# Kernel optimization log

Measured on AMD Instinct MI355X. Metric: run time of the kernel, lower is better.

## Reference

```python
import jax, jax.numpy as jnp
import numpy as np

B, C, H, W = 8, 256, 64, 64
GROUPS = 16
EPS = 1e-6


def setup_inputs() -> dict:
    key = jax.random.key(0)
    ks = jax.random.split(key, 11)
    s = 1.0 / np.sqrt(C)
    return {
        "x": jax.random.normal(ks[0], (B, C, H, W), dtype=jnp.float32),
        "norm_w": jnp.ones((C,), dtype=jnp.float32),
        "norm_b": jnp.zeros((C,), dtype=jnp.float32),
        "wq": jax.random.normal(ks[1], (C, C), dtype=jnp.float32) * s,
        "bq": jnp.zeros((C,), dtype=jnp.float32),
        "wk": jax.random.normal(ks[2], (C, C), dtype=jnp.float32) * s,
        "bk": jnp.zeros((C,), dtype=jnp.float32),
        "wv": jax.random.normal(ks[3], (C, C), dtype=jnp.float32) * s,
        "bv": jnp.zeros((C,), dtype=jnp.float32),
        "wp": jax.random.normal(ks[4], (C, C), dtype=jnp.float32) * s,
        "bp": jnp.zeros((C,), dtype=jnp.float32),
    }


def _conv1x1(h, w, b):
    # 1x1 conv == per-pixel linear over channels; w: [out_c, in_c]
    return jnp.einsum('bchw,oc->bohw', h, w) + b[None, :, None, None]


def reference(x, norm_w, norm_b, wq, bq, wk, bk, wv, bv, wp, bp):
    b, c, h, w = x.shape
    n = h * w
    # GroupNorm(16 groups, eps=1e-6, affine)
    xg = x.reshape(b, GROUPS, c // GROUPS, h, w)
    mu = xg.mean(axis=(2, 3, 4), keepdims=True)
    var = xg.var(axis=(2, 3, 4), keepdims=True)
    hn = ((xg - mu) * jax.lax.rsqrt(var + EPS)).reshape(b, c, h, w)
    hn = hn * norm_w[None, :, None, None] + norm_b[None, :, None, None]
    # QKV via 1x1 convs
    q = _conv1x1(hn, wq, bq).reshape(b, c, n)  # b c n
    k = _conv1x1(hn, wk, bk).reshape(b, c, n)
    v = _conv1x1(hn, wv, bv).reshape(b, c, n)
    # attention: scores [b, n, n], softmax over keys (last axis)
    att = jnp.einsum('bci,bcj->bij', q, k) * (c ** -0.5)
    att = jax.nn.softmax(att, axis=2)
    # h_[b,c,i] = sum_j v[b,c,j] * att[b,i,j]
    out = jnp.einsum('bcj,bij->bci', v, att).reshape(b, c, h, w)
    return x + _conv1x1(out, wp, bp)
```

## Files before the change

kernel.cpp:

```cpp
#include <hip/hip_runtime.h>


#define B_ 8
#define C_ 256
#define NPIX 4096

typedef short short8v __attribute__((ext_vector_type(8)));
typedef unsigned short ush4 __attribute__((ext_vector_type(4)));
typedef float f32x16 __attribute__((ext_vector_type(16)));

__device__ __forceinline__ unsigned short f2bf(float f) {
  unsigned u = __builtin_bit_cast(unsigned, f);
  u += 0x7fffu + ((u >> 16) & 1u);
  return (unsigned short)(u >> 16);
}

__device__ __forceinline__ void gload_lds16(const void* g, void* l) {
  __builtin_amdgcn_global_load_lds((const __attribute__((address_space(1))) void*)g,
                                   (__attribute__((address_space(3))) void*)l, 16, 0, 0);
}

__global__ __launch_bounds__(256)
void gn_part(const float4* __restrict__ x4, float* __restrict__ part) {
  const int bg = blockIdx.x >> 3;
  const int sl = blockIdx.x & 7;
  const float4* xp = x4 + (size_t)bg * (16 * NPIX / 4) + sl * 128;
  float s = 0.f, ss = 0.f;
  #pragma unroll
  for (int u = 0; u < 8; ++u) {
    const int idx = u * 256 + threadIdx.x;
    float4 v = xp[(size_t)(idx >> 7) * (NPIX / 4) + (idx & 127)];
    s  += v.x + v.y + v.z + v.w;
    ss += v.x * v.x + v.y * v.y + v.z * v.z + v.w * v.w;
  }
  #pragma unroll
  for (int off = 32; off; off >>= 1) { s += __shfl_down(s, off); ss += __shfl_down(ss, off); }
  __shared__ float sm1[4], sm2[4];
  const int w = threadIdx.x >> 6, l = threadIdx.x & 63;
  if (l == 0) { sm1[w] = s; sm2[w] = ss; }
  __syncthreads();
  if (threadIdx.x == 0) {
    part[blockIdx.x * 2]     = sm1[0] + sm1[1] + sm1[2] + sm1[3];
    part[blockIdx.x * 2 + 1] = sm2[0] + sm2[1] + sm2[2] + sm2[3];
  }
}

__global__ __launch_bounds__(128)
void gn_fin(const float* __restrict__ part, float* __restrict__ stats) {
  const int t = threadIdx.x;
  float s = 0.f, ss = 0.f;
  #pragma unroll
  for (int p = 0; p < 8; ++p) { s += part[(t * 8 + p) * 2]; ss += part[(t * 8 + p) * 2 + 1]; }
  const float mean = s * (1.f / 65536.f);
  const float var  = ss * (1.f / 65536.f) - mean * mean;
  stats[t * 2]     = mean;
  stats[t * 2 + 1] = rsqrtf(var + 1e-6f);
}

template <int MODE>
__global__ __launch_bounds__(256, 2)
void gemm_k(const float* __restrict__ Wa, const float* __restrict__ ba,
            const float* __restrict__ Wb, const float* __restrict__ bb,
            const float* __restrict__ x, const float* __restrict__ stats,
            const float* __restrict__ gamma, const float* __restrict__ beta,
            const unsigned short* __restrict__ aT,
            unsigned short* __restrict__ dq, unsigned short* __restrict__ dk,
            float* __restrict__ dout) {
  extern __shared__ __align__(16) unsigned char sm[];
  unsigned char* sX = sm;
  unsigned char* sW = sm + 32768;
  float* sscl = (float*)(sm + 65536);
  float* ssh  = sscl + 256;

  const int t = threadIdx.x;
  const int w = t >> 6, l = t & 63, hi = l >> 5, ln = l & 31;
  const int b  = blockIdx.z;
  const int n0 = blockIdx.x * 128;
  const int o0 = blockIdx.y * 128;

  const float* Wsel = (MODE == 0 && o0 >= 256) ? Wb : Wa;
  const float* bsel = (MODE == 0 && o0 >= 256) ? bb : ba;
  const int orow0 = o0 & 255;

  if (MODE < 2) {
    const int c = t;
    const float mean = stats[(b * 16 + (c >> 4)) * 2];
    const float rstd = stats[(b * 16 + (c >> 4)) * 2 + 1];
    const float sl = rstd * gamma[c];
    sscl[c] = sl; ssh[c] = beta[c] - mean * sl;
  }
  __syncthreads();

  const float* xb = x + (size_t)b * C_ * NPIX;
  const unsigned short* aTb = aT + (size_t)b * NPIX * C_;

  auto stage = [&](int s) {
    const int c0 = s * 64;
    unsigned char* Xb_ = sX + (s & 1) * 16384;
    unsigned char* Wb_ = sW + (s & 1) * 16384;
    #pragma unroll
    for (int i = 0; i < 8; ++i) {
      const int idx = i * 256 + t;
      const int o = idx >> 4;
      const int cq = (idx & 15) * 4;
      float4 v = *(const float4*)&Wsel[(size_t)(orow0 + o) * C_ + c0 + cq];
      ush4 h; h[0] = f2bf(v.x); h[1] = f2bf(v.y); h[2] = f2bf(v.z); h[3] = f2bf(v.w);
      *(ush4*)(Wb_ + ((o * 128 + cq * 2) ^ ((o & 7) << 4))) = h;
    }
    if (MODE < 2) {
      const int co = t & 7, q = t >> 3;
      float vv[8][4];
      #pragma unroll
      for (int i = 0; i < 8; ++i) {
        const int c = c0 + 8 * co + i;
        float4 v = *(const float4*)&xb[(size_t)c * NPIX + n0 + 4 * q];
        const float slc = sscl[c], shc = ssh[c];
        vv[i][0] = v.x * slc + shc; vv[i][1] = v.y * slc + shc;
        vv[i][2] = v.z * slc + shc; vv[i][3] = v.w * slc + shc;
      }
      #pragma unroll
      for (int nn = 0; nn < 4; ++nn) {
        short8v h;
        #pragma unroll
        for (int j = 0; j < 8; ++j) h[j] = (short)f2bf(vv[j][nn]);
        const int n = 4 * q + nn;
        *(short8v*)(Xb_ + ((n * 128 + 16 * co) ^ ((n & 7) << 4))) = h;
      }
    } else {
      const int cs = t & 7, nb = t >> 3;
      #pragma unroll
      for (int r = 0; r < 4; ++r) {
        const int n = nb + 32 * r;
        short8v v = *(const short8v*)&aTb[(size_t)(n0 + n) * C_ + c0 + 8 * cs];
        *(short8v*)(Xb_ + ((n * 128 + 16 * cs) ^ ((n & 7) << 4))) = v;
      }
    }
  };

  f32x16 acc[2][2];
  #pragma unroll
  for (int i = 0; i < 2; ++i)
    #pragma unroll
    for (int j = 0; j < 2; ++j)
      #pragma unroll
      for (int r = 0; r < 16; ++r) acc[i][j][r] = 0.f;

  stage(0);
  __syncthreads();
  for (int s = 0; s < 4; ++s) {
    if (s < 3) stage(s + 1);
    const unsigned char* Xb_ = sX + (s & 1) * 16384;
    const unsigned char* Wb_ = sW + (s & 1) * 16384;
    #pragma unroll
    for (int ks = 0; ks < 4; ++ks) {
      short8v xa[2], wf[2];
      #pragma unroll
      for (int mt = 0; mt < 2; ++mt) {
        const int n = 64 * (w >> 1) + 32 * mt + ln;
        xa[mt] = *(const short8v*)(Xb_ + ((n * 128 + 32 * ks + 16 * hi) ^ ((n & 7) << 4)));
        const int o = 64 * (w & 1) + 32 * mt + ln;
        wf[mt] = *(const short8v*)(Wb_ + ((o * 128 + 32 * ks + 16 * hi) ^ ((o & 7) << 4)));
      }
      #pragma unroll
      for (int mt = 0; mt < 2; ++mt)
        #pragma unroll
        for (int nt = 0; nt < 2; ++nt)
          acc[mt][nt] = (MODE == 0)
            ? __builtin_amdgcn_mfma_f32_32x32x16_bf16(xa[mt], wf[nt], acc[mt][nt], 0, 0, 0)
            : __builtin_amdgcn_mfma_f32_32x32x16_bf16(wf[mt], xa[nt], acc[mt][nt], 0, 0, 0);
    }
    __syncthreads();
  }

  if (MODE == 0) {
    unsigned short* dst = (o0 < 256) ? dq : dk;
    const float scv = (o0 < 256) ? 0.0625f : 1.0f;
    #pragma unroll
    for (int nt = 0; nt < 2; ++nt) {
      const int o = o0 + 64 * (w & 1) + 32 * nt + ln;
      const float bi = bsel[o & 255];
      #pragma unroll
      for (int mt = 0; mt < 2; ++mt)
        #pragma unroll
        for (int r = 0; r < 16; ++r) {
          const int n = n0 + 64 * (w >> 1) + 32 * mt + (r & 3) + 8 * (r >> 2) + 4 * hi;
          dst[((size_t)b * NPIX + n) * C_ + (o & 255)] = f2bf((acc[mt][nt][r] + bi) * scv);
        }
    }
  } else if (MODE == 1) {
    #pragma unroll
    for (int nt = 0; nt < 2; ++nt) {
      const int n = n0 + 64 * (w >> 1) + 32 * nt + ln;
      #pragma unroll
      for (int mt = 0; mt < 2; ++mt)
        #pragma unroll
        for (int r = 0; r < 16; ++r) {
          const int o = o0 + 64 * (w & 1) + 32 * mt + (r & 3) + 8 * (r >> 2) + 4 * hi;
          dq[((size_t)b * C_ + o) * NPIX + n] = f2bf(acc[mt][nt][r] + ba[o]);
        }
    }
  } else {
    #pragma unroll
    for (int nt = 0; nt < 2; ++nt) {
      const int n = n0 + 64 * (w >> 1) + 32 * nt + ln;
      #pragma unroll
      for (int mt = 0; mt < 2; ++mt)
        #pragma unroll
        for (int r = 0; r < 16; ++r) {
          const int o = o0 + 64 * (w & 1) + 32 * mt + (r & 3) + 8 * (r >> 2) + 4 * hi;
          const size_t ad = ((size_t)b * C_ + o) * NPIX + n;
          dout[ad] = acc[mt][nt][r] + ba[o] + x[ad];
        }
    }
  }
}

__global__ __launch_bounds__(256, 1)
void attn_k(const unsigned short* __restrict__ qt,
            const unsigned short* __restrict__ kt,
            const unsigned short* __restrict__ vb,
            unsigned short* __restrict__ aT) {
  extern __shared__ __align__(16) unsigned char smem[];
  const int t = threadIdx.x;
  const int w = t >> 6, l = t & 63, hi = l >> 5, ln = l & 31;
  const int bid = blockIdx.x;
  const int b = bid & 7;
  const int i0 = (bid >> 3) * 128;

  const size_t nc = (size_t)NPIX * C_;
  const unsigned short* qb  = qt + (size_t)b * nc;
  const unsigned char*  kbb = (const unsigned char*)(kt + (size_t)b * nc);
  const unsigned char*  vbb = (const unsigned char*)(vb + (size_t)b * nc);

  const unsigned short* qrow = qb + (size_t)(i0 + 32 * w + ln) * C_ + 8 * hi;
  short8v qf[16];
  #pragma unroll
  for (int cs = 0; cs < 16; ++cs) qf[cs] = *(const short8v*)(qrow + 16 * cs);

  f32x16 Ot[8];
  #pragma unroll
  for (int ct = 0; ct < 8; ++ct)
    #pragma unroll
    for (int r = 0; r < 16; ++r) Ot[ct][r] = 0.f;
  float m_r = -3.0e38f, l_r = 0.f;

  auto stage = [&](int buf, int j0) {
    unsigned char* Kd = smem + buf * 32768;
    unsigned char* Vd = smem + 65536 + buf * 32768;
    #pragma unroll
    for (int u = 0; u < 8; ++u) {
      const int p = w * 8192 + u * 1024 + l * 16;
      const int j = p >> 9;
      const int inner = (p & 511) ^ ((j & 7) << 4);
      gload_lds16(kbb + (size_t)(j0 + j) * 512 + inner, Kd + w * 8192 + u * 1024);
    }
    #pragma unroll
    for (int u = 0; u < 8; ++u) {
      const int p = w * 8192 + u * 1024 + l * 16;
      const int c = p >> 7;
      const int inner = (p & 127) ^ ((c & 7) << 4);
      gload_lds16(vbb + (size_t)c * 8192 + j0 * 2 + inner, Vd + w * 8192 + u * 1024);
    }
  };

  stage(0, 0);
  __syncthreads();

  for (int it = 0; it < 64; ++it) {
    const int cur = it & 1;
    if (it < 63) stage(cur ^ 1, (it + 1) * 64);

    const unsigned char* Kb = smem + cur * 32768;
    f32x16 st0, st1;
    #pragma unroll
    for (int r = 0; r < 16; ++r) { st0[r] = 0.f; st1[r] = 0.f; }
    #pragma unroll
    for (int cs = 0; cs < 16; ++cs) {
      const int cb = 32 * cs + 16 * hi;
      short8v kf0 = *(const short8v*)(Kb + ((ln * 512 + cb) ^ ((ln & 7) << 4)));
      st0 = __builtin_amdgcn_mfma_f32_32x32x16_bf16(kf0, qf[cs], st0, 0, 0, 0);
      short8v kf1 = *(const short8v*)(Kb + (((32 + ln) * 512 + cb) ^ ((ln & 7) << 4)));
      st1 = __builtin_amdgcn_mfma_f32_32x32x16_bf16(kf1, qf[cs], st1, 0, 0, 0);
    }

    float mt = st0[0];
    #pragma unroll
    for (int r = 1; r < 16; ++r) mt = fmaxf(mt, st0[r]);
    #pragma unroll
    for (int r = 0; r < 16; ++r) mt = fmaxf(mt, st1[r]);
    mt = fmaxf(mt, __shfl_xor(mt, 32));
    const float mnew = fmaxf(m_r, mt);
    const float sc = __expf(m_r - mnew);
    m_r = mnew;
    float rs = 0.f;
    #pragma unroll
    for (int r = 0; r < 16; ++r) { st0[r] = __expf(st0[r] - mnew); rs += st0[r]; }
    #pragma unroll
    for (int r = 0; r < 16; ++r) { st1[r] = __expf(st1[r] - mnew); rs += st1[r]; }
    rs += __shfl_xor(rs, 32);
    l_r = l_r * sc + rs;
    #pragma unroll
    for (int ct = 0; ct < 8; ++ct) Ot[ct] *= sc;

    short8v pf[4];
    #pragma unroll
    for (int g = 0; g < 4; ++g) {
      f32x16 sv = (g < 2) ? st0 : st1;
      const int rb = (g & 1) * 8;
      unsigned pk01, pk23, pk45, pk67;
      asm("v_cvt_pk_bf16_f32 %0, %1, %2" : "=v"(pk01) : "v"(sv[rb + 0]), "v"(sv[rb + 1]));
      asm("v_cvt_pk_bf16_f32 %0, %1, %2" : "=v"(pk23) : "v"(sv[rb + 2]), "v"(sv[rb + 3]));
      asm("v_cvt_pk_bf16_f32 %0, %1, %2" : "=v"(pk45) : "v"(sv[rb + 4]), "v"(sv[rb + 5]));
      asm("v_cvt_pk_bf16_f32 %0, %1, %2" : "=v"(pk67) : "v"(sv[rb + 6]), "v"(sv[rb + 7]));
      asm volatile("v_permlane32_swap_b32 %0, %1" : "+v"(pk01), "+v"(pk45));
      asm volatile("v_permlane32_swap_b32 %0, %1" : "+v"(pk23), "+v"(pk67));
      int4 fi = {(int)pk01, (int)pk23, (int)pk45, (int)pk67};
      pf[g] = __builtin_bit_cast(short8v, fi);
    }

    const unsigned char* Vbuf = smem + 65536 + cur * 32768;
    #pragma unroll
    for (int ks = 0; ks < 4; ++ks) {
      #pragma unroll
      for (int ct = 0; ct < 8; ++ct) {
        const int c = 32 * ct + ln;
        short8v vf = *(const short8v*)(Vbuf + ((c * 128 + 32 * ks + 16 * hi) ^ ((c & 7) << 4)));
        Ot[ct] = __builtin_amdgcn_mfma_f32_32x32x16_bf16(vf, pf[ks], Ot[ct], 0, 0, 0);
      }
    }
    __syncthreads();
  }

  const float rinv = 1.0f / l_r;
  const int iloc = 32 * w + ln;
  #pragma unroll
  for (int ct = 0; ct < 8; ++ct) {
    #pragma unroll
    for (int h = 0; h < 2; ++h) {
      const int rb = h * 8;
      unsigned pk01, pk23, pk45, pk67;
      float q0 = Ot[ct][rb + 0] * rinv, q1 = Ot[ct][rb + 1] * rinv;
      float q2 = Ot[ct][rb + 2] * rinv, q3 = Ot[ct][rb + 3] * rinv;
      float q4 = Ot[ct][rb + 4] * rinv, q5 = Ot[ct][rb + 5] * rinv;
      float q6 = Ot[ct][rb + 6] * rinv, q7 = Ot[ct][rb + 7] * rinv;
      asm("v_cvt_pk_bf16_f32 %0, %1, %2" : "=v"(pk01) : "v"(q0), "v"(q1));
      asm("v_cvt_pk_bf16_f32 %0, %1, %2" : "=v"(pk23) : "v"(q2), "v"(q3));
      asm("v_cvt_pk_bf16_f32 %0, %1, %2" : "=v"(pk45) : "v"(q4), "v"(q5));
      asm("v_cvt_pk_bf16_f32 %0, %1, %2" : "=v"(pk67) : "v"(q6), "v"(q7));
      asm volatile("v_permlane32_swap_b32 %0, %1" : "+v"(pk01), "+v"(pk45));
      asm volatile("v_permlane32_swap_b32 %0, %1" : "+v"(pk23), "+v"(pk67));
      int4 fi = {(int)pk01, (int)pk23, (int)pk45, (int)pk67};
      const int byte = (iloc * 512 + 64 * ct + 32 * h + 16 * hi) ^ ((iloc & 7) << 4);
      *(short8v*)(smem + byte) = __builtin_bit_cast(short8v, fi);
    }
  }
  __syncthreads();
  unsigned char* aTb = (unsigned char*)(aT + ((size_t)b * NPIX + i0) * C_);
  #pragma unroll
  for (int p = 0; p < 16; ++p) {
    const int idx = p * 256 + t;
    const int il = idx >> 5, ch = idx & 31;
    const int byte = (il * 512 + ch * 16) ^ ((il & 7) << 4);
    *(short8v*)(aTb + il * 512 + ch * 16) = *(const short8v*)(smem + byte);
  }
}

extern "C" void kernel_launch(void* const* d_in, const int* in_sizes, int n_in,
                              void* d_out, int out_size, void* d_ws, size_t ws_size,
                              hipStream_t stream) {
  (void)in_sizes; (void)n_in; (void)out_size; (void)ws_size;
  const float* x      = (const float*)d_in[0];
  const float* norm_w = (const float*)d_in[1];
  const float* norm_b = (const float*)d_in[2];
  const float* wq = (const float*)d_in[3];
  const float* bq = (const float*)d_in[4];
  const float* wk = (const float*)d_in[5];
  const float* bk = (const float*)d_in[6];
  const float* wv = (const float*)d_in[7];
  const float* bv = (const float*)d_in[8];
  const float* wp = (const float*)d_in[9];
  const float* bp = (const float*)d_in[10];
  float* out = (float*)d_out;

  unsigned char* ws = (unsigned char*)d_ws;
  float* part  = (float*)ws;
  float* stats = (float*)(ws + 8192);
  unsigned short* qtb = (unsigned short*)(ws + 65536);
  unsigned short* ktb = qtb + (size_t)8 * 1024 * 1024;
  unsigned short* vbb = ktb + (size_t)8 * 1024 * 1024;
  unsigned short* aTb = vbb + (size_t)8 * 1024 * 1024;

  hipFuncSetAttribute((const void*)gemm_k<0>, hipFuncAttributeMaxDynamicSharedMemorySize, 67584);
  hipFuncSetAttribute((const void*)gemm_k<1>, hipFuncAttributeMaxDynamicSharedMemorySize, 67584);
  hipFuncSetAttribute((const void*)gemm_k<2>, hipFuncAttributeMaxDynamicSharedMemorySize, 67584);
  hipFuncSetAttribute((const void*)attn_k,    hipFuncAttributeMaxDynamicSharedMemorySize, 131072);

  gn_part<<<1024, 256, 0, stream>>>((const float4*)x, part);
  gn_fin<<<1, 128, 0, stream>>>(part, stats);

  gemm_k<0><<<dim3(32, 4, B_), 256, 67584, stream>>>(wq, bq, wk, bk, x, stats, norm_w, norm_b,
                                                     nullptr, qtb, ktb, nullptr);
  gemm_k<1><<<dim3(32, 2, B_), 256, 67584, stream>>>(wv, bv, nullptr, nullptr, x, stats, norm_w, norm_b,
                                                     nullptr, vbb, nullptr, nullptr);

  attn_k<<<256, 256, 131072, stream>>>(qtb, ktb, vbb, aTb);

  gemm_k<2><<<dim3(32, 2, B_), 256, 67584, stream>>>(wp, bp, nullptr, nullptr, x, nullptr, nullptr, nullptr,
                                                     aTb, nullptr, nullptr, out);
}
```

Baseline: 392.7 us.

## Split attention over key halves, fuse QKV GEMMs, add combine kernel

The Q/K/V projections now run in one kernel, and their outputs are staged through LDS so global stores are coalesced. Attention splits the key range into two halves (512 blocks, 2 blocks/CU, smaller K/V tiles). It switches to exp2 with log2e folded into the Q scale and skips the output rescale when the running max grows by less than a threshold. A new combine kernel merges the partial outputs and writes the bf16 transposed result, aiming to fill the GPU better. The cost is an extra fp32 partial-output round trip through memory and one more kernel launch.

```diff
diff --git a/kernel.cpp b/kernel.cpp
--- a/kernel.cpp
+++ b/kernel.cpp
@@ -7,6 +7,7 @@
 
 typedef short short8v __attribute__((ext_vector_type(8)));
 typedef unsigned short ush4 __attribute__((ext_vector_type(4)));
+typedef unsigned short ush8 __attribute__((ext_vector_type(8)));
 typedef float f32x16 __attribute__((ext_vector_type(16)));
 
 __device__ __forceinline__ unsigned short f2bf(float f) {
@@ -57,15 +58,14 @@
   stats[t * 2 + 1] = rsqrtf(var + 1e-6f);
 }
 
-template <int MODE>
 __global__ __launch_bounds__(256, 2)
-void gemm_k(const float* __restrict__ Wa, const float* __restrict__ ba,
-            const float* __restrict__ Wb, const float* __restrict__ bb,
-            const float* __restrict__ x, const float* __restrict__ stats,
-            const float* __restrict__ gamma, const float* __restrict__ beta,
-            const unsigned short* __restrict__ aT,
-            unsigned short* __restrict__ dq, unsigned short* __restrict__ dk,
-            float* __restrict__ dout) {
+void qkv_k(const float* __restrict__ wq, const float* __restrict__ bq,
+           const float* __restrict__ wk, const float* __restrict__ bk,
+           const float* __restrict__ wv, const float* __restrict__ bv,
+           const float* __restrict__ x, const float* __restrict__ stats,
+           const float* __restrict__ gamma, const float* __restrict__ beta,
+           unsigned short* __restrict__ qt, unsigned short* __restrict__ kt,
+           unsigned short* __restrict__ vo) {
   extern __shared__ __align__(16) unsigned char sm[];
   unsigned char* sX = sm;
   unsigned char* sW = sm + 32768;
@@ -76,13 +76,13 @@
   const int w = t >> 6, l = t & 63, hi = l >> 5, ln = l & 31;
   const int b  = blockIdx.z;
   const int n0 = blockIdx.x * 128;
-  const int o0 = blockIdx.y * 128;
-
-  const float* Wsel = (MODE == 0 && o0 >= 256) ? Wb : Wa;
-  const float* bsel = (MODE == 0 && o0 >= 256) ? bb : ba;
-  const int orow0 = o0 & 255;
-
-  if (MODE < 2) {
+  const int y  = blockIdx.y;
+  const bool vmode = (y >= 4);
+  const float* W   = (y < 2) ? wq : ((y < 4) ? wk : wv);
+  const float* bia = (y < 2) ? bq : ((y < 4) ? bk : bv);
+  const int o0 = (y & 1) * 128;
+
+  {
     const int c = t;
     const float mean = stats[(b * 16 + (c >> 4)) * 2];
     const float rstd = stats[(b * 16 + (c >> 4)) * 2 + 1];
@@ -92,7 +92,6 @@
   __syncthreads();
 
   const float* xb = x + (size_t)b * C_ * NPIX;
-  const unsigned short* aTb = aT + (size_t)b * NPIX * C_;
 
   auto stage = [&](int s) {
     const int c0 = s * 64;
@@ -103,37 +102,27 @@
       const int idx = i * 256 + t;
       const int o = idx >> 4;
       const int cq = (idx & 15) * 4;
-      float4 v = *(const float4*)&Wsel[(size_t)(orow0 + o) * C_ + c0 + cq];
+      float4 v = *(const float4*)&W[(size_t)(o0 + o) * C_ + c0 + cq];
       ush4 h; h[0] = f2bf(v.x); h[1] = f2bf(v.y); h[2] = f2bf(v.z); h[3] = f2bf(v.w);
       *(ush4*)(Wb_ + ((o * 128 + cq * 2) ^ ((o & 7) << 4))) = h;
     }
-    if (MODE < 2) {
-      const int co = t & 7, q = t >> 3;
-      float vv[8][4];
-      #pragma unroll
-      for (int i = 0; i < 8; ++i) {
-        const int c = c0 + 8 * co + i;
-        float4 v = *(const float4*)&xb[(size_t)c * NPIX + n0 + 4 * q];
-        const float slc = sscl[c], shc = ssh[c];
-        vv[i][0] = v.x * slc + shc; vv[i][1] = v.y * slc + shc;
-        vv[i][2] = v.z * slc + shc; vv[i][3] = v.w * slc + shc;
-      }
-      #pragma unroll
-      for (int nn = 0; nn < 4; ++nn) {
-        short8v h;
-        #pragma unroll
-        for (int j = 0; j < 8; ++j) h[j] = (short)f2bf(vv[j][nn]);
-        const int n = 4 * q + nn;
-        *(short8v*)(Xb_ + ((n * 128 + 16 * co) ^ ((n & 7) << 4))) = h;
-      }
-    } else {
-      const int cs = t & 7, nb = t >> 3;
-      #pragma unroll
-      for (int r = 0; r < 4; ++r) {
-        const int n = nb + 32 * r;
-        short8v v = *(const short8v*)&aTb[(size_t)(n0 + n) * C_ + c0 + 8 * cs];
-        *(short8v*)(Xb_ + ((n * 128 + 16 * cs) ^ ((n & 7) << 4))) = v;
-      }
+    const int co = t & 7, q = t >> 3;
+    float vv[8][4];
+    #pragma unroll
+    for (int i = 0; i < 8; ++i) {
+      const int c = c0 + 8 * co + i;
+      float4 v = *(const float4*)&xb[(size_t)c * NPIX + n0 + 4 * q];
+      const float slc = sscl[c], shc = ssh[c];
+      vv[i][0] = v.x * slc + shc; vv[i][1] = v.y * slc + shc;
+      vv[i][2] = v.z * slc + shc; vv[i][3] = v.w * slc + shc;
+    }
+    #pragma unroll
+    for (int nn = 0; nn < 4; ++nn) {
+      short8v h;
+      #pragma unroll
+      for (int j = 0; j < 8; ++j) h[j] = (short)f2bf(vv[j][nn]);
+      const int n = 4 * q + nn;
+      *(short8v*)(Xb_ + ((n * 128 + 16 * co) ^ ((n & 7) << 4))) = h;
     }
   };
 
@@ -161,71 +150,77 @@
         const int o = 64 * (w & 1) + 32 * mt + ln;
         wf[mt] = *(const short8v*)(Wb_ + ((o * 128 + 32 * ks + 16 * hi) ^ ((o & 7) << 4)));
       }
-      #pragma unroll
-      for (int mt = 0; mt < 2; ++mt)
+      if (!vmode) {
         #pragma unroll
-        for (int nt = 0; nt < 2; ++nt)
-          acc[mt][nt] = (MODE == 0)
-            ? __builtin_amdgcn_mfma_f32_32x32x16_bf16(xa[mt], wf[nt], acc[mt][nt], 0, 0, 0)
-            : __builtin_amdgcn_mfma_f32_32x32x16_bf16(wf[mt], xa[nt], acc[mt][nt], 0, 0, 0);
+        for (int mt = 0; mt < 2; ++mt)
+          #pragma unroll
+          for (int nt = 0; nt < 2; ++nt)
+            acc[mt][nt] = __builtin_amdgcn_mfma_f32_32x32x16_bf16(xa[mt], wf[nt], acc[mt][nt], 0, 0, 0);
+      } else {
+        #pragma unroll
+        for (int mt = 0; mt < 2; ++mt)
+          #pragma unroll
+          for (int nt = 0; nt < 2; ++nt)
+            acc[mt][nt] = __builtin_amdgcn_mfma_f32_32x32x16_bf16(wf[mt], xa[nt], acc[mt][nt], 0, 0, 0);
+      }
     }
     __syncthreads();
   }
 
-  if (MODE == 0) {
-    unsigned short* dst = (o0 < 256) ? dq : dk;
-    const float scv = (o0 < 256) ? 0.0625f : 1.0f;
-    #pragma unroll
-    for (int nt = 0; nt < 2; ++nt) {
-      const int o = o0 + 64 * (w & 1) + 32 * nt + ln;
-      const float bi = bsel[o & 255];
-      #pragma unroll
-      for (int mt = 0; mt < 2; ++mt)
-        #pragma unroll
-        for (int r = 0; r < 16; ++r) {
-          const int n = n0 + 64 * (w >> 1) + 32 * mt + (r & 3) + 8 * (r >> 2) + 4 * hi;
-          dst[((size_t)b * NPIX + n) * C_ + (o & 255)] = f2bf((acc[mt][nt][r] + bi) * scv);
+  unsigned short* tile = (unsigned short*)sm;
+  const float qsc = (y < 2) ? (0.0625f * 1.44269504088896340736f) : 1.0f;
+  #pragma unroll
+  for (int mt = 0; mt < 2; ++mt)
+    #pragma unroll
+    for (int nt = 0; nt < 2; ++nt)
+      #pragma unroll
+      for (int r = 0; r < 16; ++r) {
+        const int crow = (r & 3) + 8 * (r >> 2) + 4 * hi;
+        int R, L; float val;
+        if (!vmode) {
+          R = 64 * (w >> 1) + 32 * mt + crow;
+          L = 64 * (w & 1) + 32 * nt + ln;
+          val = (acc[mt][nt][r] + bia[o0 + L]) * qsc;
+        } else {
+          R = 64 * (w & 1) + 32 * mt + crow;
+          L = 64 * (w >> 1) + 32 * nt + ln;
+          val = acc[mt][nt][r] + bia[o0 + R];
         }
-    }
-  } else if (MODE == 1) {
-    #pragma unroll
-    for (int nt = 0; nt < 2; ++nt) {
-      const int n = n0 + 64 * (w >> 1) + 32 * nt + ln;
-      #pragma unroll
-      for (int mt = 0; mt < 2; ++mt)
-        #pragma unroll
-        for (int r = 0; r < 16; ++r) {
-          const int o = o0 + 64 * (w & 1) + 32 * mt + (r & 3) + 8 * (r >> 2) + 4 * hi;
-          dq[((size_t)b * C_ + o) * NPIX + n] = f2bf(acc[mt][nt][r] + ba[o]);
-        }
+        tile[R * 128 + L] = f2bf(val);
+      }
+  __syncthreads();
+  if (!vmode) {
+    unsigned short* dst = ((y < 2) ? qt : kt) + ((size_t)b * NPIX + n0) * C_ + o0;
+    #pragma unroll
+    for (int u = 0; u < 8; ++u) {
+      const int idx = u * 256 + t;
+      const int R = idx >> 4, cb = idx & 15;
+      *(ush8*)(dst + (size_t)R * C_ + cb * 8) = *(const ush8*)&tile[R * 128 + cb * 8];
     }
   } else {
-    #pragma unroll
-    for (int nt = 0; nt < 2; ++nt) {
-      const int n = n0 + 64 * (w >> 1) + 32 * nt + ln;
-      #pragma unroll
-      for (int mt = 0; mt < 2; ++mt)
-        #pragma unroll
-        for (int r = 0; r < 16; ++r) {
-          const int o = o0 + 64 * (w & 1) + 32 * mt + (r & 3) + 8 * (r >> 2) + 4 * hi;
-          const size_t ad = ((size_t)b * C_ + o) * NPIX + n;
-          dout[ad] = acc[mt][nt][r] + ba[o] + x[ad];
-        }
-    }
-  }
-}
-
-__global__ __launch_bounds__(256, 1)
+    unsigned short* dst = vo + ((size_t)b * C_ + o0) * NPIX + n0;
+    #pragma unroll
+    for (int u = 0; u < 8; ++u) {
+      const int idx = u * 256 + t;
+      const int R = idx >> 4, cb = idx & 15;
+      *(ush8*)(dst + (size_t)R * NPIX + cb * 8) = *(const ush8*)&tile[R * 128 + cb * 8];
+    }
+  }
+}
+
+__global__ __launch_bounds__(256, 2)
 void attn_k(const unsigned short* __restrict__ qt,
             const unsigned short* __restrict__ kt,
             const unsigned short* __restrict__ vb,
-            unsigned short* __restrict__ aT) {
+            float* __restrict__ pO, float* __restrict__ pml) {
   extern __shared__ __align__(16) unsigned char smem[];
   const int t = threadIdx.x;
   const int w = t >> 6, l = t & 63, hi = l >> 5, ln = l & 31;
   const int bid = blockIdx.x;
-  const int b = bid & 7;
-  const int i0 = (bid >> 3) * 128;
+  const int b   = bid & 7;
+  const int jh  = (bid >> 3) & 1;
+  const int i0  = (bid >> 4) * 128;
+  const int jbase = jh * 2048;
 
   const size_t nc = (size_t)NPIX * C_;
   const unsigned short* qb  = qt + (size_t)b * nc;
@@ -245,123 +240,218 @@
   float m_r = -3.0e38f, l_r = 0.f;
 
   auto stage = [&](int buf, int j0) {
-    unsigned char* Kd = smem + buf * 32768;
-    unsigned char* Vd = smem + 65536 + buf * 32768;
-    #pragma unroll
-    for (int u = 0; u < 8; ++u) {
-      const int p = w * 8192 + u * 1024 + l * 16;
-      const int j = p >> 9;
-      const int inner = (p & 511) ^ ((j & 7) << 4);
-      gload_lds16(kbb + (size_t)(j0 + j) * 512 + inner, Kd + w * 8192 + u * 1024);
-    }
-    #pragma unroll
-    for (int u = 0; u < 8; ++u) {
-      const int p = w * 8192 + u * 1024 + l * 16;
-      const int c = p >> 7;
-      const int inner = (p & 127) ^ ((c & 7) << 4);
-      gload_lds16(vbb + (size_t)c * 8192 + j0 * 2 + inner, Vd + w * 8192 + u * 1024);
+    unsigned char* Kd = smem + buf * 16384;
+    unsigned char* Vd = smem + 32768 + buf * 16384;
+    #pragma unroll
+    for (int u = 0; u < 4; ++u) {
+      const int idx = u * 256 + t;
+      gload_lds16(kbb + (size_t)(j0 + (idx & 31)) * 512 + (idx >> 5) * 16, Kd + idx * 16);
+    }
+    #pragma unroll
+    for (int u = 0; u < 4; ++u) {
+      const int idx = u * 256 + t;
+      gload_lds16(vbb + (size_t)(idx & 255) * 8192 + j0 * 2 + (idx >> 8) * 16, Vd + idx * 16);
     }
   };
 
-  stage(0, 0);
+  stage(0, jbase);
   __syncthreads();
 
   for (int it = 0; it < 64; ++it) {
     const int cur = it & 1;
-    if (it < 63) stage(cur ^ 1, (it + 1) * 64);
-
-    const unsigned char* Kb = smem + cur * 32768;
-    f32x16 st0, st1;
-    #pragma unroll
-    for (int r = 0; r < 16; ++r) { st0[r] = 0.f; st1[r] = 0.f; }
+    if (it < 63) stage(cur ^ 1, jbase + (it + 1) * 32);
+
+    const unsigned char* Kb = smem + cur * 16384;
+    f32x16 st;
+    #pragma unroll
+    for (int r = 0; r < 16; ++r) st[r] = 0.f;
     #pragma unroll
     for (int cs = 0; cs < 16; ++cs) {
-      const int cb = 32 * cs + 16 * hi;
-      short8v kf0 = *(const short8v*)(Kb + ((ln * 512 + cb) ^ ((ln & 7) << 4)));
-      st0 = __builtin_amdgcn_mfma_f32_32x32x16_bf16(kf0, qf[cs], st0, 0, 0, 0);
-      short8v kf1 = *(const short8v*)(Kb + (((32 + ln) * 512 + cb) ^ ((ln & 7) << 4)));
-      st1 = __builtin_amdgcn_mfma_f32_32x32x16_bf16(kf1, qf[cs], st1, 0, 0, 0);
-    }
-
-    float mt = st0[0];
-    #pragma unroll
-    for (int r = 1; r < 16; ++r) mt = fmaxf(mt, st0[r]);
-    #pragma unroll
-    for (int r = 0; r < 16; ++r) mt = fmaxf(mt, st1[r]);
-    mt = fmaxf(mt, __shfl_xor(mt, 32));
-    const float mnew = fmaxf(m_r, mt);
-    const float sc = __expf(m_r - mnew);
-    m_r = mnew;
+      const short8v kf = *(const short8v*)(Kb + ((2 * cs + hi) * 32 + ln) * 16);
+      st = __builtin_amdgcn_mfma_f32_32x32x16_bf16(kf, qf[cs], st, 0, 0, 0);
+    }
+
+    float pmax = st[0];
+    #pragma unroll
+    for (int r = 1; r < 16; ++r) pmax = fmaxf(pmax, st[r]);
+    pmax = fmaxf(pmax, __shfl_xor(pmax, 32));
+    if (!__all(pmax <= m_r + 8.f)) {
+      const float mnew = fmaxf(m_r, pmax);
+      const float scf = exp2f(m_r - mnew);
+      #pragma unroll
+      for (int ct = 0; ct < 8; ++ct) Ot[ct] *= scf;
+      l_r *= scf; m_r = mnew;
+    }
     float rs = 0.f;
     #pragma unroll
-    for (int r = 0; r < 16; ++r) { st0[r] = __expf(st0[r] - mnew); rs += st0[r]; }
-    #pragma unroll
-    for (int r = 0; r < 16; ++r) { st1[r] = __expf(st1[r] - mnew); rs += st1[r]; }
+    for (int r = 0; r < 16; ++r) { st[r] = exp2f(st[r] - m_r); rs += st[r]; }
     rs += __shfl_xor(rs, 32);
-    l_r = l_r * sc + rs;
-    #pragma unroll
-    for (int ct = 0; ct < 8; ++ct) Ot[ct] *= sc;
-
-    short8v pf[4];
-    #pragma unroll
-    for (int g = 0; g < 4; ++g) {
-      f32x16 sv = (g < 2) ? st0 : st1;
-      const int rb = (g & 1) * 8;
-      unsigned pk01, pk23, pk45, pk67;
-      asm("v_cvt_pk_bf16_f32 %0, %1, %2" : "=v"(pk01) : "v"(sv[rb + 0]), "v"(sv[rb + 1]));
-      asm("v_cvt_pk_bf16_f32 %0, %1, %2" : "=v"(pk23) : "v"(sv[rb + 2]), "v"(sv[rb + 3]));
-      asm("v_cvt_pk_bf16_f32 %0, %1, %2" : "=v"(pk45) : "v"(sv[rb + 4]), "v"(sv[rb + 5]));
-      asm("v_cvt_pk_bf16_f32 %0, %1, %2" : "=v"(pk67) : "v"(sv[rb + 6]), "v"(sv[rb + 7]));
-      asm volatile("v_permlane32_swap_b32 %0, %1" : "+v"(pk01), "+v"(pk45));
-      asm volatile("v_permlane32_swap_b32 %0, %1" : "+v"(pk23), "+v"(pk67));
-      int4 fi = {(int)pk01, (int)pk23, (int)pk45, (int)pk67};
-      pf[g] = __builtin_bit_cast(short8v, fi);
-    }
-
-    const unsigned char* Vbuf = smem + 65536 + cur * 32768;
+    l_r += rs;
+
+    unsigned pk[8];
+    #pragma unroll
+    for (int p = 0; p < 8; ++p)
+      asm("v_cvt_pk_bf16_f32 %0, %1, %2" : "=v"(pk[p]) : "v"(st[2 * p]), "v"(st[2 * p + 1]));
+    asm volatile("v_permlane32_swap_b32 %0, %1" : "+v"(pk[0]), "+v"(pk[2]));
+    asm volatile("v_permlane32_swap_b32 %0, %1" : "+v"(pk[1]), "+v"(pk[3]));
+    asm volatile("v_permlane32_swap_b32 %0, %1" : "+v"(pk[4]), "+v"(pk[6]));
+    asm volatile("v_permlane32_swap_b32 %0, %1" : "+v"(pk[5]), "+v"(pk[7]));
+    int4 fA = {(int)pk[0], (int)pk[1], (int)pk[2], (int)pk[3]};
+    int4 fB = {(int)pk[4], (int)pk[5], (int)pk[6], (int)pk[7]};
+    const short8v pfA = __builtin_bit_cast(short8v, fA);
+    const short8v pfB = __builtin_bit_cast(short8v, fB);
+
+    const unsigned char* Vbuf = smem + 32768 + cur * 16384;
+    #pragma unroll
+    for (int ks = 0; ks < 2; ++ks) {
+      const short8v pf = ks ? pfB : pfA;
+      #pragma unroll
+      for (int ct = 0; ct < 8; ++ct) {
+        const short8v vf = *(const short8v*)(Vbuf + ((2 * ks + hi) * 256 + 32 * ct + ln) * 16);
+        Ot[ct] = __builtin_amdgcn_mfma_f32_32x32x16_bf16(vf, pf, Ot[ct], 0, 0, 0);
+      }
+    }
+    __syncthreads();
+  }
+
+  const size_t hb = (size_t)jh * 8 + b;
+  float* po = pO + hb * 256 * (size_t)NPIX;
+  const int i = i0 + 32 * w + ln;
+  #pragma unroll
+  for (int ct = 0; ct < 8; ++ct)
+    #pragma unroll
+    for (int r = 0; r < 16; ++r) {
+      const int c = 32 * ct + (r & 3) + 8 * (r >> 2) + 4 * hi;
+      po[(size_t)c * NPIX + i] = Ot[ct][r];
+    }
+  if (hi == 0) {
+    pml[(hb * NPIX + i) * 2 + 0] = m_r;
+    pml[(hb * NPIX + i) * 2 + 1] = l_r;
+  }
+}
+
+__global__ __launch_bounds__(256)
+void comb_k(const float* __restrict__ pO, const float* __restrict__ pml,
+            unsigned short* __restrict__ aT) {
+  __shared__ __align__(16) unsigned char tile[32768];
+  const int b  = blockIdx.y;
+  const int i0 = blockIdx.x * 64;
+  const int t  = threadIdx.x;
+  const int i  = t & 63, cq = t >> 6;
+  const size_t HALF = (size_t)8 * 256 * NPIX;
+
+  const float m0 = pml[(((size_t)0 * 8 + b) * NPIX + i0 + i) * 2 + 0];
+  const float l0 = pml[(((size_t)0 * 8 + b) * NPIX + i0 + i) * 2 + 1];
+  const float m1 = pml[(((size_t)1 * 8 + b) * NPIX + i0 + i) * 2 + 0];
+  const float l1 = pml[(((size_t)1 * 8 + b) * NPIX + i0 + i) * 2 + 1];
+  const float M  = fmaxf(m0, m1);
+  float w0 = exp2f(m0 - M), w1 = exp2f(m1 - M);
+  const float rd = 1.0f / (w0 * l0 + w1 * l1);
+  w0 *= rd; w1 *= rd;
+
+  #pragma unroll 8
+  for (int cc = 0; cc < 64; cc += 2) {
+    const int c = cq * 64 + cc;
+    const size_t off = ((size_t)b * 256 + c) * NPIX + i0 + i;
+    const float va = pO[off] * w0 + pO[off + HALF] * w1;
+    const float vbv = pO[off + NPIX] * w0 + pO[off + HALF + NPIX] * w1;
+    unsigned pkv;
+    asm("v_cvt_pk_bf16_f32 %0, %1, %2" : "=v"(pkv) : "v"(va), "v"(vbv));
+    *(unsigned*)(tile + ((i * 512 + c * 2) ^ ((i & 7) << 4))) = pkv;
+  }
+  __syncthreads();
+  unsigned short* dst = aT + ((size_t)b * NPIX + i0) * C_;
+  #pragma unroll
+  for (int u = 0; u < 8; ++u) {
+    const int idx = u * 256 + t;
+    const int ii = idx >> 5, cw = idx & 31;
+    *(ush8*)(dst + (size_t)ii * C_ + cw * 8) =
+        *(const ush8*)(tile + ((ii * 512 + cw * 16) ^ ((ii & 7) << 4)));
+  }
+}
+
+__global__ __launch_bounds__(256, 2)
+void proj_k(const float* __restrict__ Wp, const float* __restrict__ bp,
+            const float* __restrict__ x, const unsigned short* __restrict__ aT,
+            float* __restrict__ dout) {
+  extern __shared__ __align__(16) unsigned char sm[];
+  unsigned char* sX = sm;
+  unsigned char* sW = sm + 32768;
+
+  const int t = threadIdx.x;
+  const int w = t >> 6, l = t & 63, hi = l >> 5, ln = l & 31;
+  const int b  = blockIdx.z;
+  const int n0 = blockIdx.x * 128;
+  const int o0 = blockIdx.y * 128;
+
+  const unsigned short* aTb = aT + (size_t)b * NPIX * C_;
+
+  auto stage = [&](int s) {
+    const int c0 = s * 64;
+    unsigned char* Xb_ = sX + (s & 1) * 16384;
+    unsigned char* Wb_ = sW + (s & 1) * 16384;
+    #pragma unroll
+    for (int i = 0; i < 8; ++i) {
+      const int idx = i * 256 + t;
+      const int o = idx >> 4;
+      const int cq = (idx & 15) * 4;
+      float4 v = *(const float4*)&Wp[(size_t)(o0 + o) * C_ + c0 + cq];
+      ush4 h; h[0] = f2bf(v.x); h[1] = f2bf(v.y); h[2] = f2bf(v.z); h[3] = f2bf(v.w);
+      *(ush4*)(Wb_ + ((o * 128 + cq * 2) ^ ((o & 7) << 4))) = h;
+    }
+    const int cs = t & 7, nb = t >> 3;
+    #pragma unroll
+    for (int r = 0; r < 4; ++r) {
+      const int n = nb + 32 * r;
+      short8v v = *(const short8v*)&aTb[(size_t)(n0 + n) * C_ + c0 + 8 * cs];
+      *(short8v*)(Xb_ + ((n * 128 + 16 * cs) ^ ((n & 7) << 4))) = v;
+    }
+  };
+
+  f32x16 acc[2][2];
+  #pragma unroll
+  for (int i = 0; i < 2; ++i)
+    #pragma unroll
+    for (int j = 0; j < 2; ++j)
+      #pragma unroll
+      for (int r = 0; r < 16; ++r) acc[i][j][r] = 0.f;
+
+  stage(0);
+  __syncthreads();
+  for (int s = 0; s < 4; ++s) {
+    if (s < 3) stage(s + 1);
+    const unsigned char* Xb_ = sX + (s & 1) * 16384;
+    const unsigned char* Wb_ = sW + (s & 1) * 16384;
     #pragma unroll
     for (int ks = 0; ks < 4; ++ks) {
-      #pragma unroll
-      for (int ct = 0; ct < 8; ++ct) {
-        const int c = 32 * ct + ln;
-        short8v vf = *(const short8v*)(Vbuf + ((c * 128 + 32 * ks + 16 * hi) ^ ((c & 7) << 4)));
-        Ot[ct] = __builtin_amdgcn_mfma_f32_32x32x16_bf16(vf, pf[ks], Ot[ct], 0, 0, 0);
+      short8v xa[2], wf[2];
+      #pragma unroll
+      for (int mt = 0; mt < 2; ++mt) {
+        const int n = 64 * (w >> 1) + 32 * mt + ln;
+        xa[mt] = *(const short8v*)(Xb_ + ((n * 128 + 32 * ks + 16 * hi) ^ ((n & 7) << 4)));
+        const int o = 64 * (w & 1) + 32 * mt + ln;
+        wf[mt] = *(const short8v*)(Wb_ + ((o * 128 + 32 * ks + 16 * hi) ^ ((o & 7) << 4)));
       }
+      #pragma unroll
+      for (int mt = 0; mt < 2; ++mt)
+        #pragma unroll
+        for (int nt = 0; nt < 2; ++nt)
+          acc[mt][nt] = __builtin_amdgcn_mfma_f32_32x32x16_bf16(wf[mt], xa[nt], acc[mt][nt], 0, 0, 0);
     }
     __syncthreads();
   }
 
-  const float rinv = 1.0f / l_r;
-  const int iloc = 32 * w + ln;
-  #pragma unroll
-  for (int ct = 0; ct < 8; ++ct) {
-    #pragma unroll
-    for (int h = 0; h < 2; ++h) {
-      const int rb = h * 8;
-      unsigned pk01, pk23, pk45, pk67;
-      float q0 = Ot[ct][rb + 0] * rinv, q1 = Ot[ct][rb + 1] * rinv;
-      float q2 = Ot[ct][rb + 2] * rinv, q3 = Ot[ct][rb + 3] * rinv;
-      float q4 = Ot[ct][rb + 4] * rinv, q5 = Ot[ct][rb + 5] * rinv;
-      float q6 = Ot[ct][rb + 6] * rinv, q7 = Ot[ct][rb + 7] * rinv;
-      asm("v_cvt_pk_bf16_f32 %0, %1, %2" : "=v"(pk01) : "v"(q0), "v"(q1));
-      asm("v_cvt_pk_bf16_f32 %0, %1, %2" : "=v"(pk23) : "v"(q2), "v"(q3));
-      asm("v_cvt_pk_bf16_f32 %0, %1, %2" : "=v"(pk45) : "v"(q4), "v"(q5));
-      asm("v_cvt_pk_bf16_f32 %0, %1, %2" : "=v"(pk67) : "v"(q6), "v"(q7));
-      asm volatile("v_permlane32_swap_b32 %0, %1" : "+v"(pk01), "+v"(pk45));
-      asm volatile("v_permlane32_swap_b32 %0, %1" : "+v"(pk23), "+v"(pk67));
-      int4 fi = {(int)pk01, (int)pk23, (int)pk45, (int)pk67};
-      const int byte = (iloc * 512 + 64 * ct + 32 * h + 16 * hi) ^ ((iloc & 7) << 4);
-      *(short8v*)(smem + byte) = __builtin_bit_cast(short8v, fi);
-    }
-  }
-  __syncthreads();
-  unsigned char* aTb = (unsigned char*)(aT + ((size_t)b * NPIX + i0) * C_);
-  #pragma unroll
-  for (int p = 0; p < 16; ++p) {
-    const int idx = p * 256 + t;
-    const int il = idx >> 5, ch = idx & 31;
-    const int byte = (il * 512 + ch * 16) ^ ((il & 7) << 4);
-    *(short8v*)(aTb + il * 512 + ch * 16) = *(const short8v*)(smem + byte);
+  #pragma unroll
+  for (int nt = 0; nt < 2; ++nt) {
+    const int n = n0 + 64 * (w >> 1) + 32 * nt + ln;
+    #pragma unroll
+    for (int mt = 0; mt < 2; ++mt)
+      #pragma unroll
+      for (int r = 0; r < 16; ++r) {
+        const int o = o0 + 64 * (w & 1) + 32 * mt + (r & 3) + 8 * (r >> 2) + 4 * hi;
+        const size_t ad = ((size_t)b * C_ + o) * NPIX + n;
+        dout[ad] = acc[mt][nt][r] + bp[o] + x[ad];
+      }
   }
 }
 
@@ -385,26 +475,27 @@
   unsigned char* ws = (unsigned char*)d_ws;
   float* part  = (float*)ws;
   float* stats = (float*)(ws + 8192);
+  const size_t M16 = (size_t)16 * 1024 * 1024;
   unsigned short* qtb = (unsigned short*)(ws + 65536);
-  unsigned short* ktb = qtb + (size_t)8 * 1024 * 1024;
-  unsigned short* vbb = ktb + (size_t)8 * 1024 * 1024;
-  unsigned short* aTb = vbb + (size_t)8 * 1024 * 1024;
-
-  hipFuncSetAttribute((const void*)gemm_k<0>, hipFuncAttributeMaxDynamicSharedMemorySize, 67584);
-  hipFuncSetAttribute((const void*)gemm_k<1>, hipFuncAttributeMaxDynamicSharedMemorySize, 67584);
-  hipFuncSetAttribute((const void*)gemm_k<2>, hipFuncAttributeMaxDynamicSharedMemorySize, 67584);
-  hipFuncSetAttribute((const void*)attn_k,    hipFuncAttributeMaxDynamicSharedMemorySize, 131072);
+  unsigned short* ktb = (unsigned short*)(ws + 65536 + M16);
+  unsigned short* vbb = (unsigned short*)(ws + 65536 + 2 * M16);
+  unsigned short* aTb = (unsigned short*)(ws + 65536 + 3 * M16);
+  float* pO  = (float*)(ws + 65536 + 4 * M16);
+  float* pml = (float*)(ws + 65536 + 8 * M16);
+
+  hipFuncSetAttribute((const void*)qkv_k,  hipFuncAttributeMaxDynamicSharedMemorySize, 67584);
+  hipFuncSetAttribute((const void*)attn_k, hipFuncAttributeMaxDynamicSharedMemorySize, 65536);
+  hipFuncSetAttribute((const void*)proj_k, hipFuncAttributeMaxDynamicSharedMemorySize, 67584);
 
   gn_part<<<1024, 256, 0, stream>>>((const float4*)x, part);
   gn_fin<<<1, 128, 0, stream>>>(part, stats);
 
-  gemm_k<0><<<dim3(32, 4, B_), 256, 67584, stream>>>(wq, bq, wk, bk, x, stats, norm_w, norm_b,
-                                                     nullptr, qtb, ktb, nullptr);
-  gemm_k<1><<<dim3(32, 2, B_), 256, 67584, stream>>>(wv, bv, nullptr, nullptr, x, stats, norm_w, norm_b,
-                                                     nullptr, vbb, nullptr, nullptr);
-
-  attn_k<<<256, 256, 131072, stream>>>(qtb, ktb, vbb, aTb);
-
-  gemm_k<2><<<dim3(32, 2, B_), 256, 67584, stream>>>(wp, bp, nullptr, nullptr, x, nullptr, nullptr, nullptr,
-                                                     aTb, nullptr, nullptr, out);
-}
+  qkv_k<<<dim3(32, 6, B_), 256, 67584, stream>>>(wq, bq, wk, bk, wv, bv, x, stats,
+                                                 norm_w, norm_b, qtb, ktb, vbb);
+
+  attn_k<<<512, 256, 65536, stream>>>(qtb, ktb, vbb, pO, pml);
+
+  comb_k<<<dim3(NPIX / 64, B_), 256, 0, stream>>>(pO, pml, aTb);
+
+  proj_k<<<dim3(32, 2, B_), 256, 67584, stream>>>(wp, bp, x, aTb, out);
+}
```

New measurement: 345.9 us. -11.9%, faster.
